# Kernel optimization log

Measured on AMD Instinct MI355X. Metric: run time of the kernel, lower is better.

The kernel has to match this reference:

```python
import jax, jax.numpy as jnp
import numpy as np

N_HEADS = 16
EPS = 1e-12  # torch F.normalize eps


def srmsnorm(x):
    # F.normalize(x, dim=-1) * sqrt(dim)
    d = x.shape[-1]
    norm = jnp.sqrt(jnp.sum(x * x, axis=-1, keepdims=True))
    return x / jnp.maximum(norm, EPS) * jnp.sqrt(jnp.float32(d))


def setup_inputs() -> dict:
    key = jax.random.key(0)
    ks = jax.random.split(key, 7)
    B, S, D, F = 2, 2048, 1024, 4096
    x = jax.random.normal(ks[0], (B, S, D), dtype=jnp.float32)
    # xavier-uniform-ish scale for square weights
    lim = np.sqrt(6.0 / (D + D)).astype(np.float32)
    wq = jax.random.uniform(ks[1], (D, D), jnp.float32, -lim, lim)
    wk = jax.random.uniform(ks[2], (D, D), jnp.float32, -lim, lim)
    wv = jax.random.uniform(ks[3], (D, D), jnp.float32, -lim, lim)
    wo = jax.random.uniform(ks[4], (D, D), jnp.float32, -lim, lim)
    w_in = jax.random.normal(ks[5], (D, F), dtype=jnp.float32) * np.sqrt(2.0 / D).astype(np.float32)
    lim2 = np.sqrt(6.0 / (D + F)).astype(np.float32)
    w_out = jax.random.uniform(ks[6], (F, D), jnp.float32, -lim2, lim2)
    return {"x": x, "wq": wq, "wk": wk, "wv": wv, "wo": wo, "w_in": w_in, "w_out": w_out}


def attention(x, wq, wk, wv, wo):
    B, S, D = x.shape
    H = N_HEADS
    hd = D // H
    scale = hd ** -0.5
    q = (x @ wq).reshape(B, S, H, hd).transpose(0, 2, 1, 3)  # [B,H,S,hd]
    k = (x @ wk).reshape(B, S, H, hd).transpose(0, 2, 1, 3)
    v = (x @ wv).reshape(B, S, H, hd).transpose(0, 2, 1, 3)
    scores = jnp.einsum('bhqd,bhkd->bhqk', q, k) * scale  # [B,H,S,S]
    causal = jnp.tril(jnp.ones((S, S), dtype=bool))
    scores = jnp.where(causal, scores, jnp.float32(-jnp.inf))
    probs = jax.nn.softmax(scores, axis=-1)
    out = jnp.einsum('bhqk,bhkd->bhqd', probs, v)  # [B,H,S,hd]
    out = out.transpose(0, 2, 1, 3).reshape(B, S, D)
    return out @ wo


def reference(x, wq, wk, wv, wo, w_in, w_out):
    h = x + attention(srmsnorm(x), wq, wk, wv, wo)
    ff = jax.nn.gelu(srmsnorm(h) @ w_in, approximate=True) @ w_out
    return h + ff
```

## Files before the change

### kernel.cpp

```cpp
#include <hip/hip_runtime.h>
#include <math.h>

#define BB 2
#define SS 2048
#define DD 1024
#define FF 4096
#define HH 16
#define MM (BB * SS)

typedef __attribute__((ext_vector_type(8))) short short8v;
typedef __attribute__((ext_vector_type(4))) float float4v;
typedef __attribute__((ext_vector_type(4))) unsigned short ushort4v;
typedef __attribute__((ext_vector_type(8))) unsigned short ushort8v;
typedef unsigned short u16;
typedef unsigned int u32;

#define MFMA16(A_, B_, C_) __builtin_amdgcn_mfma_f32_16x16x32_bf16((A_), (B_), (C_), 0, 0, 0)

__device__ __forceinline__ u16 f2bf(float f) {
    u32 u = __float_as_uint(f);
    u += 0x7FFF + ((u >> 16) & 1);
    return (u16)(u >> 16);
}

__device__ __forceinline__ void async16(void* lds, const void* g) {
    __builtin_amdgcn_global_load_lds(
        (const __attribute__((address_space(1))) u32*)g,
        (__attribute__((address_space(3))) u32*)lds, 16, 0, 0);
}

__device__ __forceinline__ float gelu_f(float x) {
    float u = 0.7978845608028654f * x * (1.0f + 0.044715f * x * x);
    float e = exp2f(u * 2.8853900817779268f);
    float th = 1.0f - 2.0f / (e + 1.0f);
    return 0.5f * x * (1.0f + th);
}

__global__ __launch_bounds__(256) void srmsnorm_bf16(const float* __restrict__ in,
                                                     u16* __restrict__ out) {
    const int row = blockIdx.x, t = threadIdx.x;
    float4 a = reinterpret_cast<const float4*>(in + (size_t)row * DD)[t];
    float ss = a.x * a.x + a.y * a.y + a.z * a.z + a.w * a.w;
#pragma unroll
    for (int off = 32; off > 0; off >>= 1) ss += __shfl_xor(ss, off);
    __shared__ float red[4];
    if ((t & 63) == 0) red[t >> 6] = ss;
    __syncthreads();
    float tot = red[0] + red[1] + red[2] + red[3];
    float sc = 32.0f / fmaxf(sqrtf(tot), 1e-12f);
    ushort4v ov;
    ov[0] = f2bf(a.x * sc); ov[1] = f2bf(a.y * sc);
    ov[2] = f2bf(a.z * sc); ov[3] = f2bf(a.w * sc);
    *(ushort4v*)(out + (size_t)row * DD + t * 4) = ov;
}

__device__ __forceinline__ void trans_tile(const float* __restrict__ in,
                                           u16* __restrict__ out, int K, int N,
                                           int n0, int k0, int t, float (*T)[65]) {
#pragma unroll
    for (int i = 0; i < 4; ++i) {
        int r = i * 16 + (t >> 4), c4 = (t & 15) * 4;
        float4 v = *reinterpret_cast<const float4*>(in + (size_t)(k0 + r) * N + n0 + c4);
        T[r][c4 + 0] = v.x; T[r][c4 + 1] = v.y; T[r][c4 + 2] = v.z; T[r][c4 + 3] = v.w;
    }
    __syncthreads();
#pragma unroll
    for (int i = 0; i < 4; ++i) {
        int r = i * 16 + (t >> 4), c4 = (t & 15) * 4;
        ushort4v ov;
#pragma unroll
        for (int j = 0; j < 4; ++j) ov[j] = f2bf(T[c4 + j][r]);
        *(ushort4v*)(out + (size_t)(n0 + r) * K + k0 + c4) = ov;
    }
}

__global__ __launch_bounds__(256) void wtrans_all(const float* __restrict__ wq,
                                                  const float* __restrict__ wk,
                                                  const float* __restrict__ wv,
                                                  const float* __restrict__ wo,
                                                  const float* __restrict__ wi,
                                                  const float* __restrict__ wo2,
                                                  char* __restrict__ ws) {
    __shared__ float T[64][65];
    const int t = threadIdx.x;
    const size_t MB = 1024 * 1024;
    int id = blockIdx.x;
    if (id < 1024) {
        const int which = id >> 8, l = id & 255;
        const float* in = which == 0 ? wq : which == 1 ? wk : which == 2 ? wv : wo;
        u16* out = (u16*)(ws + (size_t)which * 2 * MB);
        trans_tile(in, out, 1024, 1024, (l & 15) * 64, (l >> 4) * 64, t, T);
    } else if (id < 2048) {
        const int l = id - 1024;
        trans_tile(wi, (u16*)(ws + 8 * MB), 1024, 4096,
                   (l & 63) * 64, (l >> 6) * 64, t, T);
    } else {
        const int l = id - 2048;
        trans_tile(wo2, (u16*)(ws + 16 * MB), 4096, 1024,
                   (l & 15) * 64, (l >> 4) * 64, t, T);
    }
}

__global__ __launch_bounds__(256) void vtrans(const u16* __restrict__ vb,
                                              u16* __restrict__ vt) {
    __shared__ u16 T[64][88];
    const int t = threadIdx.x;
    const int s0 = blockIdx.x * 64, bh = blockIdx.y;
    const int b = bh >> 4, h = bh & 15;
#pragma unroll
    for (int i = 0; i < 2; ++i) {
        int r = i * 32 + (t >> 3), c8 = (t & 7) * 8;
        *(ushort8v*)&T[r][c8] =
            *(const ushort8v*)(vb + (size_t)(b * SS + s0 + r) * DD + h * 64 + c8);
    }
    __syncthreads();
#pragma unroll
    for (int i = 0; i < 2; ++i) {
        int d = i * 32 + (t >> 3), s8 = (t & 7) * 8;
        ushort8v ov;
#pragma unroll
        for (int j = 0; j < 8; ++j) ov[j] = T[s8 + j][d];
        *(ushort8v*)(vt + ((size_t)bh * 64 + d) * SS + s0 + s8) = ov;
    }
}

template <int BM, int BN, int EPI>
__global__ __launch_bounds__(256) void gemm_bf16(const u16* __restrict__ A,
                                                 const u16* __restrict__ Bt,
                                                 const float* __restrict__ Res,
                                                 void* __restrict__ Cout,
                                                 int M, int N, int K) {
    __shared__ u16 As[BM * 32];
    __shared__ u16 Bs[BN * 32];
    constexpr int FM = BM / 32, FN = BN / 32;
    const int t = threadIdx.x;
    const int w = t >> 6, lane = t & 63;
    const int g = lane >> 4, c = lane & 15;
    const int wr = w >> 1, wc = w & 1;
    const int gx = gridDim.x;
    const int nwg = gx * gridDim.y;
    int wg = blockIdx.y * gx + blockIdx.x;
    {
        const int q = nwg >> 3, rr = nwg & 7;
        const int xcd = wg & 7, loc = wg >> 3;
        wg = (xcd < rr) ? xcd * (q + 1) + loc
                        : rr * (q + 1) + (xcd - rr) * q + loc;
    }
    const int bm = (wg / gx) * BM, bn = (wg % gx) * BN;
    const int arow = t >> 2, au = (t & 3) * 8;

    float4v acc[FM][FN] = {};
    for (int k0 = 0; k0 < K; k0 += 32) {
        __syncthreads();
#pragma unroll
        for (int p = 0; p < BM / 64; ++p)
            async16(&As[(p * 64 + arow) * 32 + au],
                    A + (size_t)(bm + p * 64 + arow) * K + k0 + au);
#pragma unroll
        for (int p = 0; p < BN / 64; ++p)
            async16(&Bs[(p * 64 + arow) * 32 + au],
                    Bt + (size_t)(bn + p * 64 + arow) * K + k0 + au);
        __syncthreads();
        short8v af[FM], bf[FN];
#pragma unroll
        for (int mi = 0; mi < FM; ++mi)
            af[mi] = *(const short8v*)&As[(wr * (BM / 2) + mi * 16 + c) * 32 + g * 8];
#pragma unroll
        for (int ni = 0; ni < FN; ++ni)
            bf[ni] = *(const short8v*)&Bs[(wc * (BN / 2) + ni * 16 + c) * 32 + g * 8];
#pragma unroll
        for (int mi = 0; mi < FM; ++mi)
#pragma unroll
            for (int ni = 0; ni < FN; ++ni)
                acc[mi][ni] = MFMA16(af[mi], bf[ni], acc[mi][ni]);
    }
    const int row0 = bm + wr * (BM / 2), col0 = bn + wc * (BN / 2);
    if (EPI == 3) {
        const int seg = col0 >> 10, c0 = col0 & 1023;
        u16* dst = (u16*)Cout + (size_t)seg * ((size_t)MM * 1024);
#pragma unroll
        for (int mi = 0; mi < FM; ++mi)
#pragma unroll
            for (int r = 0; r < 4; ++r) {
                const size_t rw = (size_t)(row0 + mi * 16 + 4 * g + r) * 1024;
#pragma unroll
                for (int ni = 0; ni < FN; ++ni)
                    dst[rw + c0 + ni * 16 + c] = f2bf(acc[mi][ni][r]);
            }
        return;
    }
#pragma unroll
    for (int mi = 0; mi < FM; ++mi)
#pragma unroll
        for (int r = 0; r < 4; ++r) {
            const size_t rw = (size_t)(row0 + mi * 16 + 4 * g + r) * N;
#pragma unroll
            for (int ni = 0; ni < FN; ++ni) {
                const size_t off = rw + col0 + ni * 16 + c;
                float v = acc[mi][ni][r];
                if (EPI == 0)      ((u16*)Cout)[off] = f2bf(v);
                else if (EPI == 1) ((float*)Cout)[off] = v + Res[off];
                else               ((u16*)Cout)[off] = f2bf(gelu_f(v));
            }
        }
}

__global__ __launch_bounds__(64) void attn_split(const u16* __restrict__ Qb,
                                                 const u16* __restrict__ Kb,
                                                 const u16* __restrict__ Vt,
                                                 float* __restrict__ po,
                                                 float* __restrict__ pml) {
    __shared__ u16 Pl[2][16][88];
    const int lane = threadIdx.x;
    const int g = lane >> 4, c = lane & 15;
    const int bid = blockIdx.x;
    const int s = bid & 1;
    const int uid = bid >> 1;
    const int bh = uid & 31;
    const int u = 63 - (uid >> 5);
    const int b = bh >> 4, h = bh & 15;
    const int qrow0 = u * 32;
    const int nkt = (u >> 1) + 1;
    const int half = (nkt + 1) >> 1;
    const int kt0 = s ? half : 0;
    const int kt1 = s ? nkt : half;
    float* myo = po + ((size_t)(uid * 2 + s)) * 32 * 64;
    float* mym = pml + ((size_t)(uid * 2 + s)) * 2 * 32;

    if (kt0 >= kt1) {
#pragma unroll
        for (int rb = 0; rb < 2; ++rb)
#pragma unroll
            for (int nb = 0; nb < 4; ++nb)
#pragma unroll
                for (int r = 0; r < 4; ++r)
                    myo[(rb * 16 + 4 * g + r) * 64 + nb * 16 + c] = 0.0f;
        if (c == 0)
#pragma unroll
            for (int rb = 0; rb < 2; ++rb)
#pragma unroll
                for (int r = 0; r < 4; ++r) {
                    mym[rb * 16 + 4 * g + r] = -1e30f;
                    mym[32 + rb * 16 + 4 * g + r] = 0.0f;
                }
        return;
    }

    const size_t qkbase = (size_t)b * SS * DD + h * 64;
    const size_t vbase = (size_t)bh * 64 * SS;
    constexpr float SC = 0.18033688011112042f;

    short8v qf[2][2];
#pragma unroll
    for (int rb = 0; rb < 2; ++rb)
#pragma unroll
        for (int kh = 0; kh < 2; ++kh)
            qf[rb][kh] = *(const short8v*)(Qb + qkbase +
                             (size_t)(qrow0 + rb * 16 + c) * DD + kh * 32 + g * 8);

    float4v o[2][4] = {};
    float m_run[2][4], l_run[2][4];
#pragma unroll
    for (int rb = 0; rb < 2; ++rb)
#pragma unroll
        for (int r = 0; r < 4; ++r) { m_run[rb][r] = -1e30f; l_run[rb][r] = 0.0f; }

    for (int kt = kt0; kt < kt1; ++kt) {
        short8v kf[4][2];
#pragma unroll
        for (int nb = 0; nb < 4; ++nb)
#pragma unroll
            for (int kh = 0; kh < 2; ++kh)
                kf[nb][kh] = *(const short8v*)(Kb + qkbase +
                                 (size_t)(kt * 64 + nb * 16 + c) * DD + kh * 32 + g * 8);
        float4v sa[2][4] = {};
        __builtin_amdgcn_s_setprio(1);
#pragma unroll
        for (int nb = 0; nb < 4; ++nb)
#pragma unroll
            for (int kh = 0; kh < 2; ++kh)
#pragma unroll
                for (int rb = 0; rb < 2; ++rb)
                    sa[rb][nb] = MFMA16(qf[rb][kh], kf[nb][kh], sa[rb][nb]);
        __builtin_amdgcn_s_setprio(0);

        const bool diag = (kt == nkt - 1);
#pragma unroll
        for (int rb = 0; rb < 2; ++rb)
#pragma unroll
            for (int nb = 0; nb < 4; ++nb)
#pragma unroll
                for (int r = 0; r < 4; ++r) {
                    float v = sa[rb][nb][r] * SC;
                    if (diag && (kt * 64 + nb * 16 + c > qrow0 + rb * 16 + 4 * g + r))
                        v = -3e38f;
                    sa[rb][nb][r] = v;
                }

#pragma unroll
        for (int rb = 0; rb < 2; ++rb) {
            float corr[4];
#pragma unroll
            for (int r = 0; r < 4; ++r) {
                float m0 = fmaxf(fmaxf(sa[rb][0][r], sa[rb][1][r]),
                                 fmaxf(sa[rb][2][r], sa[rb][3][r]));
                m0 = fmaxf(m0, __shfl_xor(m0, 1));
                m0 = fmaxf(m0, __shfl_xor(m0, 2));
                m0 = fmaxf(m0, __shfl_xor(m0, 4));
                m0 = fmaxf(m0, __shfl_xor(m0, 8));
                float mn = fmaxf(m_run[rb][r], m0);
                corr[r] = exp2f(m_run[rb][r] - mn);
                m_run[rb][r] = mn;
            }
#pragma unroll
            for (int nb = 0; nb < 4; ++nb)
#pragma unroll
                for (int r = 0; r < 4; ++r)
                    sa[rb][nb][r] = exp2f(sa[rb][nb][r] - m_run[rb][r]);
#pragma unroll
            for (int r = 0; r < 4; ++r) {
                float s_ = sa[rb][0][r] + sa[rb][1][r] + sa[rb][2][r] + sa[rb][3][r];
                s_ += __shfl_xor(s_, 1); s_ += __shfl_xor(s_, 2);
                s_ += __shfl_xor(s_, 4); s_ += __shfl_xor(s_, 8);
                l_run[rb][r] = l_run[rb][r] * corr[r] + s_;
            }
            float4v cv; cv[0] = corr[0]; cv[1] = corr[1]; cv[2] = corr[2]; cv[3] = corr[3];
#pragma unroll
            for (int nb = 0; nb < 4; ++nb) o[rb][nb] *= cv;
#pragma unroll
            for (int nb = 0; nb < 4; ++nb)
#pragma unroll
                for (int r = 0; r < 4; ++r)
                    Pl[rb][4 * g + r][nb * 16 + c] = f2bf(sa[rb][nb][r]);
        }

        short8v pa[2][2];
#pragma unroll
        for (int rb = 0; rb < 2; ++rb)
#pragma unroll
            for (int kh = 0; kh < 2; ++kh)
                pa[rb][kh] = *(const short8v*)&Pl[rb][c][kh * 32 + g * 8];
        short8v vf[4][2];
#pragma unroll
        for (int nb = 0; nb < 4; ++nb)
#pragma unroll
            for (int kh = 0; kh < 2; ++kh)
                vf[nb][kh] = *(const short8v*)(Vt + vbase +
                                 (size_t)(nb * 16 + c) * SS + kt * 64 + kh * 32 + g * 8);
        __builtin_amdgcn_s_setprio(1);
#pragma unroll
        for (int nb = 0; nb < 4; ++nb)
#pragma unroll
            for (int kh = 0; kh < 2; ++kh)
#pragma unroll
                for (int rb = 0; rb < 2; ++rb)
                    o[rb][nb] = MFMA16(pa[rb][kh], vf[nb][kh], o[rb][nb]);
        __builtin_amdgcn_s_setprio(0);
    }

#pragma unroll
    for (int rb = 0; rb < 2; ++rb)
#pragma unroll
        for (int nb = 0; nb < 4; ++nb)
#pragma unroll
            for (int r = 0; r < 4; ++r)
                myo[(rb * 16 + 4 * g + r) * 64 + nb * 16 + c] = o[rb][nb][r];
    if (c == 0)
#pragma unroll
        for (int rb = 0; rb < 2; ++rb)
#pragma unroll
            for (int r = 0; r < 4; ++r) {
                mym[rb * 16 + 4 * g + r] = m_run[rb][r];
                mym[32 + rb * 16 + 4 * g + r] = l_run[rb][r];
            }
}

__global__ __launch_bounds__(256) void attn_comb(const float* __restrict__ po,
                                                 const float* __restrict__ pml,
                                                 u16* __restrict__ Ao) {
    const int uid = blockIdx.x;
    const int bh = uid & 31;
    const int u = 63 - (uid >> 5);
    const int b = bh >> 4, h = bh & 15;
    const int qrow0 = u * 32;
    const int t = threadIdx.x;
    const int row = t >> 3, c8 = (t & 7) * 8;

    const float* ml0 = pml + (size_t)(uid * 2 + 0) * 64;
    const float* ml1 = pml + (size_t)(uid * 2 + 1) * 64;
    const float m0 = ml0[row], l0 = ml0[32 + row];
    const float m1 = ml1[row], l1 = ml1[32 + row];
    const float mm = fmaxf(m0, m1);
    const float e0 = exp2f(m0 - mm), e1 = exp2f(m1 - mm);
    const float inv = 1.0f / (e0 * l0 + e1 * l1);

    const float* o0 = po + ((size_t)(uid * 2 + 0) * 32 + row) * 64 + c8;
    const float* o1 = po + ((size_t)(uid * 2 + 1) * 32 + row) * 64 + c8;
    float4 a0 = *(const float4*)o0, b0 = *(const float4*)(o0 + 4);
    float4 a1 = *(const float4*)o1, b1 = *(const float4*)(o1 + 4);
    ushort8v ov;
    ov[0] = f2bf((e0 * a0.x + e1 * a1.x) * inv);
    ov[1] = f2bf((e0 * a0.y + e1 * a1.y) * inv);
    ov[2] = f2bf((e0 * a0.z + e1 * a1.z) * inv);
    ov[3] = f2bf((e0 * a0.w + e1 * a1.w) * inv);
    ov[4] = f2bf((e0 * b0.x + e1 * b1.x) * inv);
    ov[5] = f2bf((e0 * b0.y + e1 * b1.y) * inv);
    ov[6] = f2bf((e0 * b0.z + e1 * b1.z) * inv);
    ov[7] = f2bf((e0 * b0.w + e1 * b1.w) * inv);
    *(ushort8v*)(Ao + (size_t)b * SS * DD + (size_t)(qrow0 + row) * DD + h * 64 + c8) = ov;
}

extern "C" void kernel_launch(void* const* d_in, const int* in_sizes, int n_in,
                              void* d_out, int out_size, void* d_ws, size_t ws_size,
                              hipStream_t stream) {
    const float* x     = (const float*)d_in[0];
    const float* wq    = (const float*)d_in[1];
    const float* wk    = (const float*)d_in[2];
    const float* wv    = (const float*)d_in[3];
    const float* wo    = (const float*)d_in[4];
    const float* w_in  = (const float*)d_in[5];
    const float* w_out = (const float*)d_in[6];
    float* out = (float*)d_out;
    char* ws = (char*)d_ws;
    const size_t MB = 1024 * 1024;
    u16* wq_t  = (u16*)(ws + 0 * MB);
    u16* wo_t  = (u16*)(ws + 6 * MB);
    u16* wi_t  = (u16*)(ws + 8 * MB);
    u16* wo2_t = (u16*)(ws + 16 * MB);
    u16* xn    = (u16*)(ws + 24 * MB);
    u16* qb    = (u16*)(ws + 32 * MB);
    u16* vb    = (u16*)(ws + 48 * MB);
    u16* vt    = (u16*)(ws + 56 * MB);
    u16* ao    = (u16*)(ws + 64 * MB);
    u16* hn    = (u16*)(ws + 72 * MB);
    u16* gbuf  = (u16*)(ws + 80 * MB);
    float* po  = (float*)(ws + 80 * MB);
    float* pml = (float*)(ws + 24 * MB);

    dim3 blk(256);
    wtrans_all<<<dim3(3072), blk, 0, stream>>>(wq, wk, wv, wo, w_in, w_out, ws);

    srmsnorm_bf16<<<MM, blk, 0, stream>>>(x, xn);
    gemm_bf16<128, 128, 3><<<dim3(3072 / 128, MM / 128), blk, 0, stream>>>(
        xn, wq_t, nullptr, qb, MM, 3072, DD);
    vtrans<<<dim3(SS / 64, BB * HH), blk, 0, stream>>>(vb, vt);
    attn_split<<<dim3(32 * 64 * 2), dim3(64), 0, stream>>>(
        qb, qb + (size_t)MM * 1024, vt, po, pml);
    attn_comb<<<dim3(2048), blk, 0, stream>>>(po, pml, ao);
    gemm_bf16<128, 128, 1><<<dim3(DD / 128, MM / 128), blk, 0, stream>>>(ao, wo_t, x, out, MM, DD, DD);
    srmsnorm_bf16<<<MM, blk, 0, stream>>>(out, hn);
    gemm_bf16<128, 128, 2><<<dim3(FF / 128, MM / 128), blk, 0, stream>>>(hn, wi_t, nullptr, gbuf, MM, FF, DD);
    gemm_bf16<128, 128, 1><<<dim3(DD / 128, MM / 128), blk, 0, stream>>>(gbuf, wo2_t, out, out, MM, DD, FF);
}
```

Baseline: 418.5 us.

## Split-K the final FFN down-projection GEMM into two partials plus add kernel

The last GEMM (K=4096, output 4096x1024) previously launched only 256 workgroups, each running a long K loop. It now splits K across gridDim.z=2, giving 512 workgroups that each write fp32 partial sums to a workspace buffer. A new elementwise kernel then adds both partials plus the residual into the output. This is meant to fill the GPU's compute units better, at the cost of an extra 32 MB of fp32 partial traffic and one more kernel launch.

```diff
diff --git a/kernel.cpp b/kernel.cpp
--- a/kernel.cpp
+++ b/kernel.cpp
@@ -148,9 +148,11 @@
     }
     const int bm = (wg / gx) * BM, bn = (wg % gx) * BN;
     const int arow = t >> 2, au = (t & 3) * 8;
+    const int kseg = K / (int)gridDim.z;
+    const int kbeg = (int)blockIdx.z * kseg, kend = kbeg + kseg;
 
     float4v acc[FM][FN] = {};
-    for (int k0 = 0; k0 < K; k0 += 32) {
+    for (int k0 = kbeg; k0 < kend; k0 += 32) {
         __syncthreads();
 #pragma unroll
         for (int p = 0; p < BM / 64; ++p)
@@ -186,6 +188,19 @@
 #pragma unroll
                 for (int ni = 0; ni < FN; ++ni)
                     dst[rw + c0 + ni * 16 + c] = f2bf(acc[mi][ni][r]);
+            }
+        return;
+    }
+    if (EPI == 4) {
+        float* dst = (float*)Cout + (size_t)blockIdx.z * M * N;
+#pragma unroll
+        for (int mi = 0; mi < FM; ++mi)
+#pragma unroll
+            for (int r = 0; r < 4; ++r) {
+                const size_t rw = (size_t)(row0 + mi * 16 + 4 * g + r) * N;
+#pragma unroll
+                for (int ni = 0; ni < FN; ++ni)
+                    dst[rw + col0 + ni * 16 + c] = acc[mi][ni][r];
             }
         return;
     }
@@ -203,6 +218,17 @@
                 else               ((u16*)Cout)[off] = f2bf(gelu_f(v));
             }
         }
+}
+
+__global__ __launch_bounds__(256) void add2_f32(const float* __restrict__ p0,
+                                                const float* __restrict__ p1,
+                                                float* __restrict__ out) {
+    const size_t i = ((size_t)blockIdx.x * 256 + threadIdx.x) * 4;
+    float4 a = *(const float4*)(out + i);
+    float4 b = *(const float4*)(p0 + i);
+    float4 c = *(const float4*)(p1 + i);
+    a.x += b.x + c.x; a.y += b.y + c.y; a.z += b.z + c.z; a.w += b.w + c.w;
+    *(float4*)(out + i) = a;
 }
 
 __global__ __launch_bounds__(64) void attn_split(const u16* __restrict__ Qb,
@@ -436,6 +462,7 @@
     u16* gbuf  = (u16*)(ws + 80 * MB);
     float* po  = (float*)(ws + 80 * MB);
     float* pml = (float*)(ws + 24 * MB);
+    float* psum = (float*)(ws + 32 * MB);
 
     dim3 blk(256);
     wtrans_all<<<dim3(3072), blk, 0, stream>>>(wq, wk, wv, wo, w_in, w_out, ws);
@@ -450,5 +477,7 @@
     gemm_bf16<128, 128, 1><<<dim3(DD / 128, MM / 128), blk, 0, stream>>>(ao, wo_t, x, out, MM, DD, DD);
     srmsnorm_bf16<<<MM, blk, 0, stream>>>(out, hn);
     gemm_bf16<128, 128, 2><<<dim3(FF / 128, MM / 128), blk, 0, stream>>>(hn, wi_t, nullptr, gbuf, MM, FF, DD);
-    gemm_bf16<128, 128, 1><<<dim3(DD / 128, MM / 128), blk, 0, stream>>>(gbuf, wo2_t, out, out, MM, DD, FF);
-}
+    gemm_bf16<128, 128, 4><<<dim3(DD / 128, MM / 128, 2), blk, 0, stream>>>(
+        gbuf, wo2_t, nullptr, psum, MM, DD, FF);
+    add2_f32<<<dim3(4096), blk, 0, stream>>>(psum, psum + (size_t)MM * DD, out);
+}
```

Result: no change. 416.8 us (-0.4%).
